# Optimization experiments

Hardware: AMD Instinct MI355X
Metric: run time of the kernel (lower is better)

The kernel has to match this reference:

```python
import jax, jax.numpy as jnp
import numpy as np
import math

B, L, D_MODEL = 4, 2048, 512
EXPAND, D_STATE, D_CONV = 6, 8, 3
D_INNER = EXPAND * D_MODEL            # 3072
DT_RANK = math.ceil(D_MODEL / 16)     # 32
NH = 8
HF = D_MODEL // NH                    # 64


def setup_inputs() -> dict:
    key = jax.random.key(0)
    ks = jax.random.split(key, 16)
    n = lambda k, sh, s=0.02: jax.random.normal(k, sh, dtype=jnp.float32) * s
    return {
        "x": jax.random.normal(ks[0], (B, L, D_MODEL), dtype=jnp.float32),
        "norm_w": jnp.ones((D_MODEL,), jnp.float32),
        "in_proj_w": n(ks[1], (2 * D_INNER, D_MODEL)),
        "conv_w": n(ks[2], (D_INNER, 1, D_CONV), 0.2),
        "conv_b": jnp.zeros((D_INNER,), jnp.float32),
        "x_proj_w": n(ks[3], (DT_RANK + 2 * D_STATE, D_INNER)),
        "dt_head_w": n(ks[4], (D_INNER, DT_RANK)),
        "dt_head_b": jnp.zeros((D_INNER,), jnp.float32),
        "D": jnp.ones((D_INNER,), jnp.float32),
        "reduce_w": n(ks[5], (D_MODEL, D_INNER)),
        "q_net_w": n(ks[6], (D_MODEL, D_MODEL)),
        "gain_q_w": n(ks[7], (D_MODEL, D_MODEL)),
        "gain_k_w": n(ks[8], (D_MODEL, D_MODEL)),
        "alpha": jnp.ones((1,), jnp.float32),
        "beta": jnp.zeros((1,), jnp.float32),
        "qkv_w": n(ks[9], (3 * D_MODEL + NH, D_MODEL)),
        "qkv_b": jnp.zeros((3 * D_MODEL + NH,), jnp.float32),
        "ttt_lr_bias": jnp.zeros((NH,), jnp.float32),
        "W1": n(ks[10], (NH, HF, HF)),
        "b1": jnp.zeros((NH, HF), jnp.float32),
        "token_idx": 1.0 / jnp.arange(1, L + 1, dtype=jnp.float32),
        "token_idx_bias": jnp.zeros((L,), jnp.float32),
        "ttt_ln_w": jnp.ones((NH, HF), jnp.float32),
        "ttt_ln_b": jnp.zeros((NH, HF), jnp.float32),
        "post_norm_w": jnp.ones((D_MODEL,), jnp.float32),
        "post_norm_b": jnp.zeros((D_MODEL,), jnp.float32),
        "wo_w": n(ks[11], (D_MODEL, D_MODEL)),
        "wo_b": jnp.zeros((D_MODEL,), jnp.float32),
    }


def _rmsnorm(x, w, eps=1e-5):
    return x * jax.lax.rsqrt(jnp.mean(x * x, axis=-1, keepdims=True) + eps) * w


def _layernorm(x, w, b, eps=1e-5):
    mu = x.mean(-1, keepdims=True)
    xh = (x - mu) * jax.lax.rsqrt(x.var(-1, keepdims=True) + eps)
    return xh * w + b


def _longhorn_scan(x, z, dt, k, q, dt_b, D):
    # x,z,dt: [B,L,di]; k,q: [B,L,ds].  Online Longhorn recurrence (matches step()).
    def step(s, t):
        x_t, z_t, dt_t, k_t, q_t = t
        dt_t = jax.nn.sigmoid(dt_t + dt_b)
        dt_t = dt_t / (1.0 + dt_t * jnp.sum(k_t * k_t, -1, keepdims=True))
        dB = dt_t[:, :, None] * k_t[:, None, :]                  # [B,di,ds]
        s = s * (1.0 - dB * k_t[:, None, :]) + x_t[:, :, None] * dB
        y_t = jnp.einsum('bdn,bn->bd', s, q_t) + D * x_t
        return s, y_t * jax.nn.silu(z_t)

    s0 = jnp.zeros((x.shape[0], x.shape[2], k.shape[2]), x.dtype)
    xs = tuple(jnp.moveaxis(a, 1, 0) for a in (x, z, dt, k, q))
    _, ys = jax.lax.scan(step, s0, xs)
    return jnp.moveaxis(ys, 0, 1)                                # [B,L,di]


def _ttt(h, qkv_w, qkv_b, ttt_lr_bias, W1, b1, token_idx, token_idx_bias,
         ln_w, ln_b, pn_w, pn_b, wo_w, wo_b, lr_mult=1.0):
    Bh, N, d = h.shape
    proj = h @ qkv_w.T + qkv_b                                   # [B,N,3d+NH]
    XQK, XV, XGate, lr = (proj[..., :d], proj[..., d:2 * d],
                          proj[..., 2 * d:3 * d], proj[..., 3 * d:])

    def heads(a):  # [B,N,d] -> [B*NH,N,HF]
        return a.reshape(Bh, N, NH, HF).transpose(0, 2, 1, 3).reshape(Bh * NH, N, HF)

    XQ = heads(XQK)            # XQ == XK in the source
    XVh = heads(XV)
    ttt_lr = jax.nn.sigmoid(lr + ttt_lr_bias) * lr_mult          # [B,N,NH]
    ttt_lr = jnp.swapaxes(ttt_lr, 0, 1).reshape(N, Bh * NH, 1)   # [N,B*NH,1]
    tok = jnp.maximum(token_idx + token_idx_bias, 0.0)           # [N]

    W1c = jnp.broadcast_to(W1[None], (Bh, NH, HF, HF)).reshape(Bh * NH, HF, HF)
    b1c = jnp.broadcast_to(b1[None], (Bh, NH, HF)).reshape(Bh * NH, HF)
    lnw = jnp.broadcast_to(ln_w[None], (Bh, NH, HF)).reshape(Bh * NH, HF)
    lnb = jnp.broadcast_to(ln_b[None], (Bh, NH, HF)).reshape(Bh * NH, HF)
    eps = 1e-6
    HFf = jnp.float32(HF)

    def step(carry, t):
        W, bb = carry
        xk, xv, lr_t, tok_t = t
        Z1 = jnp.einsum('bf,bfg->bg', xk, W) + bb
        mu = Z1.mean(-1, keepdims=True)
        std = jnp.sqrt(Z1.var(-1, keepdims=True) + eps)
        xh = (Z1 - mu) / std
        # grad of ||LN(Z1) - (XV - XK)||^2 wrt Z1 (ln_fused_l2_bwd)
        go = (lnw * xh + lnb) - (xv - xk)
        gxh = go * lnw
        grad = (HFf * gxh - gxh.sum(-1, keepdims=True)
                - xh * (gxh * xh).sum(-1, keepdims=True)) / (HFf * std)
        eta = lr_t * tok_t                                       # [B*NH,1]
        W = W - eta[:, :, None] * (xk[:, :, None] * grad[:, None, :])
        bb = bb - eta * grad
        Z1q = jnp.einsum('bf,bfg->bg', xk, W) + bb
        mu2 = Z1q.mean(-1, keepdims=True)
        std2 = jnp.sqrt(Z1q.var(-1, keepdims=True) + eps)
        out_t = xk + lnw * (Z1q - mu2) / std2 + lnb
        return (W, bb), out_t

    xs = (jnp.moveaxis(XQ, 1, 0), jnp.moveaxis(XVh, 1, 0), ttt_lr, tok)
    _, ys = jax.lax.scan(step, (W1c, b1c), xs)                   # [N,B*NH,HF]
    xqw = ys.reshape(N, Bh, NH, HF).transpose(1, 0, 2, 3).reshape(Bh, N, d)
    normed = _layernorm(xqw, pn_w, pn_b)
    gated = jax.nn.gelu(XGate, approximate=True) * normed
    return gated @ wo_w.T + wo_b


def reference(x, norm_w, in_proj_w, conv_w, conv_b, x_proj_w, dt_head_w, dt_head_b,
              D, reduce_w, q_net_w, gain_q_w, gain_k_w, alpha, beta,
              qkv_w, qkv_b, ttt_lr_bias, W1, b1, token_idx, token_idx_bias,
              ttt_ln_w, ttt_ln_b, post_norm_w, post_norm_b, wo_w, wo_b):
    residual = x                                   # residual=None in forward
    xn = _rmsnorm(residual, norm_w)
    # ---- Longhorn block ----
    xz = xn @ in_proj_w.T                          # [B,L,2*di]
    xx, z = jnp.split(xz, 2, axis=-1)
    xc = jnp.swapaxes(xx, 1, 2)                    # [B,di,L]
    xc = jax.lax.conv_general_dilated(
        xc, conv_w, (1,), [(D_CONV - 1, 0)],       # causal depthwise conv
        dimension_numbers=('NCH', 'OIH', 'NCH'), feature_group_count=D_INNER)
    xc = jax.nn.silu(xc + conv_b[None, :, None])
    xb = jnp.swapaxes(xc, 1, 2)                    # [B,L,di]
    x_dbl = xb @ x_proj_w.T
    dt = x_dbl[..., :DT_RANK] @ dt_head_w.T        # [B,L,di] (bias added in scan)
    k = x_dbl[..., DT_RANK:DT_RANK + D_STATE]
    q = x_dbl[..., DT_RANK + D_STATE:]
    y = _longhorn_scan(xb, z, dt, k, q, dt_head_b, D)   # h_hidden, [B,L,di]
    # (out_proj output is discarded by PreCoBlock, so not computed)
    h_red = y @ reduce_w.T                          # [B,L,d]
    # ---- TTT corrective branch ----
    c_hidden = _ttt(h_red, qkv_w, qkv_b, ttt_lr_bias, W1, b1, token_idx,
                    token_idx_bias, ttt_ln_w, ttt_ln_b, post_norm_w, post_norm_b,
                    wo_w, wo_b, lr_mult=1.0)
    z_long = h_red @ q_net_w.T
    z_ttt = c_hidden @ q_net_w.T
    gq = h_red @ gain_q_w.T
    gk = h_red @ gain_k_w.T
    # score = mean_i (gq_i . gk_j)/sqrt(d) == (mean_i gq_i) . gk_j / sqrt(d)
    score = jnp.einsum('bd,bld->bl', gq.mean(axis=1), gk) / jnp.sqrt(jnp.float32(D_MODEL))
    gain = jnp.minimum(jax.nn.sigmoid(alpha * score + beta), 0.55)[..., None]
    out = z_long + gain * (z_ttt - z_long)
    return (out, residual, gain)
```

## Files before the change

### kernel.cpp

```cpp
#include <hip/hip_runtime.h>
#include <hip/hip_bf16.h>
#include <cstdint>
#include <cstddef>

#define L_SEQ 2048
#define BATCH 4
#define DM    512
#define DI    3072
#define NROWS (BATCH * L_SEQ)
#define PROJW 1544
#define CTILE 16
#define BDI   (BATCH * DI)
#define SB    64
#define NSB   (L_SEQ / SB)
#define CHT   16
#define LCH   128
#define NLCH  (L_SEQ / LCH)

using bf16 = __hip_bfloat16;

typedef __attribute__((ext_vector_type(8))) short short8v;
typedef __attribute__((ext_vector_type(4))) float f32x4;


__device__ __forceinline__ float sigmoidf_(float x) { return 1.f / (1.f + __expf(-x)); }
__device__ __forceinline__ float us2f(unsigned int u) {
    union { unsigned int i; float f; } c; c.i = u << 16; return c.f;
}
__device__ __forceinline__ bf16  f2b(float f) { return __float2bfloat16(f); }
__device__ __forceinline__ float b2f(bf16 v)  { return __bfloat162float(v); }
__device__ __forceinline__ void st1(float* p, float v) { *p = v; }
__device__ __forceinline__ void st1(bf16* p, float v)  { *p = f2b(v); }

template <int CTRL>
__device__ __forceinline__ float dppadd_(float x) {
    int s = __builtin_amdgcn_update_dpp(0, __builtin_bit_cast(int, x), CTRL, 0xF, 0xF, true);
    return x + __builtin_bit_cast(float, s);
}
__device__ __forceinline__ float wave_sum_u(float x) {
    x = dppadd_<0x111>(x);
    x = dppadd_<0x112>(x);
    x = dppadd_<0x114>(x);
    x = dppadd_<0x118>(x);
    x = dppadd_<0x142>(x);
    x = dppadd_<0x143>(x);
    return __builtin_bit_cast(float,
        __builtin_amdgcn_readlane(__builtin_bit_cast(int, x), 63));
}

__global__ __launch_bounds__(256) void copy4_k(const float4* __restrict__ in,
                                               float4* __restrict__ out, int n) {
    int i = blockIdx.x * 256 + threadIdx.x;
    if (i < n) out[i] = in[i];
}

__global__ __launch_bounds__(256) void cvt_k(const float* __restrict__ in,
                                             bf16* __restrict__ out, int n4) {
    int i = blockIdx.x * 256 + threadIdx.x;
    if (i >= n4) return;
    float4 v = ((const float4*)in)[i];
    out[4 * i + 0] = f2b(v.x);
    out[4 * i + 1] = f2b(v.y);
    out[4 * i + 2] = f2b(v.z);
    out[4 * i + 3] = f2b(v.w);
}

__global__ __launch_bounds__(256) void cvt3_k(const float* __restrict__ a,
                                              const float* __restrict__ b,
                                              const float* __restrict__ c,
                                              bf16* __restrict__ out) {
    int i = blockIdx.x * 256 + threadIdx.x;
    const int seg = 512 * 512 / 4;
    const float* src = (i < seg) ? a : (i < 2 * seg) ? b : c;
    int j = (i < seg) ? i : (i < 2 * seg) ? i - seg : i - 2 * seg;
    float4 v = ((const float4*)src)[j];
    bf16* o = out + (size_t)i * 4;
    o[0] = f2b(v.x); o[1] = f2b(v.y); o[2] = f2b(v.z); o[3] = f2b(v.w);
}

__global__ __launch_bounds__(256) void rmsnorm_res_k(const float* __restrict__ x,
                                                     const float* __restrict__ w,
                                                     bf16* __restrict__ xn,
                                                     float* __restrict__ res) {
    int r = blockIdx.x, tid = threadIdx.x;
    const float* row = x + (size_t)r * DM;
    float v0 = row[tid], v1 = row[tid + 256];
    float q = v0 * v0 + v1 * v1;
#pragma unroll
    for (int off = 32; off; off >>= 1) q += __shfl_xor(q, off);
    __shared__ float sm[4];
    if ((tid & 63) == 0) sm[tid >> 6] = q;
    __syncthreads();
    q = sm[0] + sm[1] + sm[2] + sm[3];
    float scale = rsqrtf(q * (1.f / 512.f) + 1e-5f);
    bf16* orow = xn + (size_t)r * DM;
    float* rrow = res + (size_t)r * DM;
    orow[tid]       = f2b(v0 * scale * w[tid]);
    orow[tid + 256] = f2b(v1 * scale * w[tid + 256]);
    rrow[tid]       = v0;
    rrow[tid + 256] = v1;
}

template <int BIAS, typename TC>
__global__ __launch_bounds__(256) void gemm_mfma(const bf16* __restrict__ A, int lda,
                                                 const bf16* __restrict__ Wb, int ldw,
                                                 const float* __restrict__ bias,
                                                 TC* __restrict__ C, int ldc,
                                                 int N, int K) {
    __shared__ __align__(16) bf16 As[128 * 48];
    __shared__ __align__(16) bf16 Ws[128 * 48];
    const int tid = threadIdx.x;
    const int lane = tid & 63;
    const int widx = tid >> 6;
    const int bm = blockIdx.x * 128;
    const int bn = blockIdx.y * 128;
    const int wr = (widx >> 1) * 64;
    const int wc = (widx & 1) * 64;

    f32x4 acc[4][4];
#pragma unroll
    for (int i = 0; i < 4; ++i)
#pragma unroll
        for (int j = 0; j < 4; ++j) acc[i][j] = (f32x4){0.f, 0.f, 0.f, 0.f};

    const int r0 = tid >> 2;
    const int c0 = tid & 3;
    const int frow = lane & 15;
    const int fk = (lane >> 4) * 8;

    int n0 = bn + r0;       if (n0 > N - 1) n0 = N - 1;
    int n1 = bn + r0 + 64;  if (n1 > N - 1) n1 = N - 1;
    const bf16* pa0 = A + (size_t)(bm + r0) * lda + c0 * 8;
    const bf16* pa1 = A + (size_t)(bm + r0 + 64) * lda + c0 * 8;
    const bf16* pb0 = Wb + (size_t)n0 * ldw + c0 * 8;
    const bf16* pb1 = Wb + (size_t)n1 * ldw + c0 * 8;

    for (int k0 = 0; k0 < K; k0 += 32) {
        short8v a0 = *(const short8v*)(pa0 + k0);
        short8v a1 = *(const short8v*)(pa1 + k0);
        short8v b0 = *(const short8v*)(pb0 + k0);
        short8v b1 = *(const short8v*)(pb1 + k0);
        __syncthreads();
        *(short8v*)&As[r0 * 48 + c0 * 8] = a0;
        *(short8v*)&As[(r0 + 64) * 48 + c0 * 8] = a1;
        *(short8v*)&Ws[r0 * 48 + c0 * 8] = b0;
        *(short8v*)&Ws[(r0 + 64) * 48 + c0 * 8] = b1;
        __syncthreads();
        short8v af[4], bg[4];
#pragma unroll
        for (int mi = 0; mi < 4; ++mi)
            af[mi] = *(const short8v*)&As[(wr + mi * 16 + frow) * 48 + fk];
#pragma unroll
        for (int ni = 0; ni < 4; ++ni)
            bg[ni] = *(const short8v*)&Ws[(wc + ni * 16 + frow) * 48 + fk];
#pragma unroll
        for (int mi = 0; mi < 4; ++mi)
#pragma unroll
            for (int ni = 0; ni < 4; ++ni)
                acc[mi][ni] = __builtin_amdgcn_mfma_f32_16x16x32_bf16(
                    af[mi], bg[ni], acc[mi][ni], 0, 0, 0);
    }

#pragma unroll
    for (int ni = 0; ni < 4; ++ni) {
        int col = bn + wc + ni * 16 + (lane & 15);
        if (col < N) {
            float bz = BIAS ? bias[col] : 0.f;
#pragma unroll
            for (int mi = 0; mi < 4; ++mi) {
                int rbase = bm + wr + mi * 16 + (lane >> 4) * 4;
#pragma unroll
                for (int r = 0; r < 4; ++r) {
                    float v = acc[mi][ni][r] + bz;
                    st1(&C[(size_t)(rbase + r) * ldc + col], v);
                }
            }
        }
    }
}

__global__ __launch_bounds__(256) void conv_boundary_k(const bf16* __restrict__ x,
                                                       bf16* __restrict__ side) {
    int idx = blockIdx.x * 256 + threadIdx.x;
    const int total = (L_SEQ / CTILE - 1) * 2 * BDI;
    if (idx >= total) return;
    int col = idx % BDI;
    int rr = idx / BDI;
    int tile = (rr >> 1) + 1;
    int r = rr & 1;
    int b = col / DI, d = col % DI;
    int l = tile * CTILE - 2 + r;
    side[idx] = x[((size_t)b * L_SEQ + l) * DI + d];
}

__global__ __launch_bounds__(256) void conv_tile_k(bf16* __restrict__ x,
                                                   const bf16* __restrict__ side,
                                                   const float* __restrict__ cw,
                                                   const float* __restrict__ cb) {
    int idx = blockIdx.x * 256 + threadIdx.x;
    const int total = (L_SEQ / CTILE) * BDI;
    if (idx >= total) return;
    int col = idx % BDI;
    int tile = idx / BDI;
    int b = col / DI, d = col % DI;
    float w0 = cw[3 * d], w1 = cw[3 * d + 1], w2 = cw[3 * d + 2], bias = cb[d];
    size_t base = ((size_t)b * L_SEQ + tile * CTILE) * DI + d;
    float xm2, xm1;
    if (tile == 0) { xm2 = 0.f; xm1 = 0.f; }
    else {
        const bf16* sp = side + ((size_t)(tile - 1) * 2) * BDI + col;
        xm2 = b2f(sp[0]);
        xm1 = b2f(sp[BDI]);
    }
    float cur = b2f(x[base]);
#pragma unroll
    for (int i = 0; i < CTILE; ++i) {
        float nxt = (i + 1 < CTILE) ? b2f(x[base + (size_t)(i + 1) * DI]) : 0.f;
        float a = bias + w0 * xm2 + w1 * xm1 + w2 * cur;
        x[base + (size_t)i * DI] = f2b(a * sigmoidf_(a));
        xm2 = xm1; xm1 = cur; cur = nxt;
    }
}

__global__ __launch_bounds__(256) void longhorn_p1(const bf16* __restrict__ xb,
                                                   const float* __restrict__ xdbl,
                                                   const float* __restrict__ dtw,
                                                   const float* __restrict__ dtb_v,
                                                   float* __restrict__ pq) {
    int idx = blockIdx.x * 256 + threadIdx.x;
    int ch = idx / BDI;
    int col = idx % BDI;
    int b = col / DI, d = col % DI;
    float w32[32];
#pragma unroll
    for (int i = 0; i < 32; ++i) w32[i] = dtw[d * 32 + i];
    float dtb = dtb_v[d];
    float P[8] = {1.f, 1.f, 1.f, 1.f, 1.f, 1.f, 1.f, 1.f};
    float Q[8] = {0.f, 0.f, 0.f, 0.f, 0.f, 0.f, 0.f, 0.f};
    size_t rbase = ((size_t)b * L_SEQ + ch * LCH) * DI + d;
    const float* xdb = xdbl + ((size_t)b * L_SEQ + ch * LCH) * 48;

    float xv = b2f(xb[rbase]);
    for (int t = 0; t < LCH; ++t) {
        float x_c = xv;
        if (t + 1 < LCH) xv = b2f(xb[rbase + (size_t)(t + 1) * DI]);
        const float* row = xdb + (size_t)t * 48;
        float dt_c = 0.f;
#pragma unroll
        for (int i = 0; i < 32; i += 4) {
            float4 r4 = *(const float4*)(row + i);
            dt_c = fmaf(r4.x, w32[i + 0], dt_c);
            dt_c = fmaf(r4.y, w32[i + 1], dt_c);
            dt_c = fmaf(r4.z, w32[i + 2], dt_c);
            dt_c = fmaf(r4.w, w32[i + 3], dt_c);
        }
        float kq[8];
#pragma unroll
        for (int i = 0; i < 8; i += 4) *(float4*)&kq[i] = *(const float4*)(row + 32 + i);
        float sig = sigmoidf_(dt_c + dtb);
        float ksq = 0.f;
#pragma unroll
        for (int n = 0; n < 8; ++n) ksq = fmaf(kq[n], kq[n], ksq);
        float dts = sig / (1.f + sig * ksq);
#pragma unroll
        for (int n = 0; n < 8; ++n) {
            float dB = dts * kq[n];
            float a = 1.f - dB * kq[n];
            P[n] *= a;
            Q[n] = fmaf(Q[n], a, x_c * dB);
        }
    }
    float* o = pq + (size_t)idx * 16;
#pragma unroll
    for (int n = 0; n < 8; n += 4) {
        *(float4*)(o + n)     = make_float4(P[n], P[n + 1], P[n + 2], P[n + 3]);
        *(float4*)(o + 8 + n) = make_float4(Q[n], Q[n + 1], Q[n + 2], Q[n + 3]);
    }
}

__global__ __launch_bounds__(256) void longhorn_p2(float* __restrict__ pq) {
    int col = blockIdx.x * 256 + threadIdx.x;
    float s[8] = {0.f, 0.f, 0.f, 0.f, 0.f, 0.f, 0.f, 0.f};
    for (int c = 0; c < NLCH; ++c) {
        float* base = pq + ((size_t)c * BDI + col) * 16;
        float P[8], Q[8];
#pragma unroll
        for (int n = 0; n < 8; n += 4) {
            *(float4*)&P[n] = *(const float4*)(base + n);
            *(float4*)&Q[n] = *(const float4*)(base + 8 + n);
        }
#pragma unroll
        for (int n = 0; n < 8; n += 4)
            *(float4*)(base + n) = make_float4(s[n], s[n + 1], s[n + 2], s[n + 3]);
#pragma unroll
        for (int n = 0; n < 8; ++n) s[n] = fmaf(P[n], s[n], Q[n]);
    }
}

__global__ __launch_bounds__(256) void longhorn_p3(bf16* __restrict__ xb_y,
                                                   const bf16* __restrict__ z,
                                                   const float* __restrict__ xdbl,
                                                   const float* __restrict__ dtw,
                                                   const float* __restrict__ dtb_v,
                                                   const float* __restrict__ Dv,
                                                   const float* __restrict__ pq) {
    int idx = blockIdx.x * 256 + threadIdx.x;
    int ch = idx / BDI;
    int col = idx % BDI;
    int b = col / DI, d = col % DI;
    float w32[32];
#pragma unroll
    for (int i = 0; i < 32; ++i) w32[i] = dtw[d * 32 + i];
    float dtb = dtb_v[d], Dd = Dv[d];
    float s[8];
    {
        const float* base = pq + (size_t)idx * 16;
#pragma unroll
        for (int n = 0; n < 8; n += 4) *(float4*)&s[n] = *(const float4*)(base + n);
    }
    size_t rbase = ((size_t)b * L_SEQ + ch * LCH) * DI + d;
    const float* xdb = xdbl + ((size_t)b * L_SEQ + ch * LCH) * 48;

    float xv = b2f(xb_y[rbase]);
    float zv = b2f(z[rbase]);
    for (int t = 0; t < LCH; ++t) {
        float x_c = xv, z_c = zv;
        if (t + 1 < LCH) {
            size_t nidx = rbase + (size_t)(t + 1) * DI;
            xv = b2f(xb_y[nidx]);
            zv = b2f(z[nidx]);
        }
        const float* row = xdb + (size_t)t * 48;
        float dt_c = 0.f;
#pragma unroll
        for (int i = 0; i < 32; i += 4) {
            float4 r4 = *(const float4*)(row + i);
            dt_c = fmaf(r4.x, w32[i + 0], dt_c);
            dt_c = fmaf(r4.y, w32[i + 1], dt_c);
            dt_c = fmaf(r4.z, w32[i + 2], dt_c);
            dt_c = fmaf(r4.w, w32[i + 3], dt_c);
        }
        float kq[16];
#pragma unroll
        for (int i = 0; i < 16; i += 4) *(float4*)&kq[i] = *(const float4*)(row + 32 + i);
        float sig = sigmoidf_(dt_c + dtb);
        float ksq = 0.f;
#pragma unroll
        for (int n = 0; n < 8; ++n) ksq = fmaf(kq[n], kq[n], ksq);
        float dts = sig / (1.f + sig * ksq);
        float y = 0.f;
#pragma unroll
        for (int n = 0; n < 8; ++n) {
            float dB = dts * kq[n];
            s[n] = s[n] * (1.f - dB * kq[n]) + x_c * dB;
            y = fmaf(s[n], kq[8 + n], y);
        }
        y = fmaf(Dd, x_c, y);
        float out = y * (z_c * sigmoidf_(z_c));
        xb_y[rbase + (size_t)t * DI] = f2b(out);
    }
}

__global__ __launch_bounds__(128) void prep_ttt_k(const bf16* __restrict__ proj,
                                                  const float* __restrict__ lr_bias,
                                                  const float* __restrict__ tok_idx,
                                                  const float* __restrict__ tok_bias,
                                                  const float* __restrict__ ln_w,
                                                  const float* __restrict__ ln_b,
                                                  float* __restrict__ xkf,
                                                  float* __restrict__ etav,
                                                  float* __restrict__ q0s) {
    int bh = blockIdx.x >> 4;
    int t = (blockIdx.x & 15) * 128 + threadIdx.x;
    int b = bh >> 3, h = bh & 7;
    const bf16* prow = proj + ((size_t)b * L_SEQ + t) * PROJW;
    const bf16* pk = prow + h * 64;
    const bf16* pv = prow + 512 + h * 64;
    const float* lwp = ln_w + h * 64;
    const float* lbp = ln_b + h * 64;
    float* xo = xkf + ((size_t)bh * L_SEQ + t) * 64;
    float q0 = 0.f;
#pragma unroll
    for (int i = 0; i < 64; i += 8) {
        short8v sk = *(const short8v*)(pk + i);
        short8v sv = *(const short8v*)(pv + i);
        float v[8];
#pragma unroll
        for (int j = 0; j < 8; ++j) {
            float xk = us2f((unsigned short)sk[j]);
            float xv = us2f((unsigned short)sv[j]);
            v[j] = xk;
            q0 = fmaf((lbp[i + j] - xv + xk), lwp[i + j], q0);
        }
        *(float4*)(xo + i)     = make_float4(v[0], v[1], v[2], v[3]);
        *(float4*)(xo + i + 4) = make_float4(v[4], v[5], v[6], v[7]);
    }
    float eta = sigmoidf_(b2f(prow[1536 + h]) + lr_bias[h]) *
                fmaxf(tok_idx[t] + tok_bias[t], 0.f);
    size_t o = (size_t)bh * L_SEQ + t;
    etav[o] = eta;
    q0s[o]  = q0;
}

__global__ __launch_bounds__(64) void gram16_k(const float* __restrict__ xkf,
                                               float* __restrict__ gram) {
    int bh = blockIdx.x >> 7, c16 = blockIdx.x & 127;
    int lane = threadIdx.x;
    __shared__ __align__(16) float xs[16][68];
    const float* src = xkf + ((size_t)bh * L_SEQ + c16 * 16) * 64;
    {
        int r = lane >> 2, cb = (lane & 3) * 16;
#pragma unroll
        for (int j = 0; j < 4; ++j)
            *(float4*)&xs[r][cb + 4 * j] = *(const float4*)(src + (size_t)r * 64 + cb + 4 * j);
    }
    __syncthreads();
    int t = lane >> 2, s0 = lane & 3;
    float* dst = gram + ((size_t)(bh * 128 + c16) * 16 + t) * 16;
#pragma unroll
    for (int jj = 0; jj < 4; ++jj) {
        int s = s0 * 4 + jj;
        float a0 = 0.f, a1 = 0.f, a2 = 0.f, a3 = 0.f;
#pragma unroll
        for (int j = 0; j < 16; ++j) {
            float4 u = *(const float4*)&xs[t][4 * j];
            float4 v = *(const float4*)&xs[s][4 * j];
            a0 = fmaf(u.x, v.x, a0); a1 = fmaf(u.y, v.y, a1);
            a2 = fmaf(u.z, v.z, a2); a3 = fmaf(u.w, v.w, a3);
        }
        dst[s] = (a0 + a1) + (a2 + a3);
    }
}

__device__ __forceinline__ void ttt_body(const bf16* __restrict__ proj,
                                         const float* __restrict__ xkf,
                                         const float* __restrict__ etav,
                                         const float* __restrict__ q0s,
                                         const float* __restrict__ gram16,
                                         const float* __restrict__ W1,
                                         const float* __restrict__ b1,
                                         const float* __restrict__ ln_w,
                                         const float* __restrict__ ln_b,
                                         bf16* __restrict__ xqw) {
    const int lane = threadIdx.x;
    const int bh = blockIdx.x;
    const int b = bh >> 3, h = bh & 7;

    __shared__ __align__(16) float xkb[2][SB][64];
    __shared__ __align__(16) bf16  xvb[2][SB][64];
    __shared__ __align__(16) float kb[2][4][CHT][CHT];
    __shared__ __align__(16) float sc[2][2][SB];
    __shared__ __align__(16) float zbb[CHT][64];
    __shared__ __align__(16) float z1qb[CHT][64];
    __shared__ __align__(16) float egb[CHT][64];
    __shared__ float mub[CHT];

    float W[64];
#pragma unroll
    for (int f = 0; f < 64; ++f) W[f] = W1[(size_t)(h * 64 + f) * 64 + lane];
    float bvec = b1[h * 64 + lane];
    float lw = ln_w[h * 64 + lane];
    float lb = ln_b[h * 64 + lane];
    float p = lw * lw;

    const float* kfg = xkf + (size_t)bh * L_SEQ * 64;
    const bf16*  pvg = proj + (size_t)b * L_SEQ * PROJW + 512 + h * 64;
    const float* evg = etav + (size_t)bh * L_SEQ;
    const float* qg  = q0s + (size_t)bh * L_SEQ;
    const float* gmg = gram16 + (size_t)bh * 128 * 256;

    auto stage_async = [&](int c, int bi) {
        const int t0g = c * SB;
#pragma unroll
        for (int i = 0; i < 16; ++i) {
            const float* gp = kfg + (size_t)(t0g + 4 * i) * 64 + lane * 4;
            __builtin_amdgcn_global_load_lds(
                (const __attribute__((address_space(1))) void*)gp,
                (__attribute__((address_space(3))) void*)&xkb[bi][4 * i][0], 16, 0, 0);
        }
#pragma unroll
        for (int i = 0; i < 8; ++i) {
            const bf16* gp = pvg + (size_t)(t0g + 8 * i + (lane >> 3)) * PROJW + (lane & 7) * 8;
            __builtin_amdgcn_global_load_lds(
                (const __attribute__((address_space(1))) void*)gp,
                (__attribute__((address_space(3))) void*)&xvb[bi][8 * i][0], 16, 0, 0);
        }
#pragma unroll
        for (int i = 0; i < 4; ++i) {
            const float* gp = gmg + (size_t)c * 1024 + i * 256 + lane * 4;
            __builtin_amdgcn_global_load_lds(
                (const __attribute__((address_space(1))) void*)gp,
                (__attribute__((address_space(3))) void*)(&kb[bi][0][0][0] + i * 256), 16, 0, 0);
        }
        {
            const float* g0 = evg + t0g + lane;
            __builtin_amdgcn_global_load_lds(
                (const __attribute__((address_space(1))) void*)g0,
                (__attribute__((address_space(3))) void*)&sc[bi][0][0], 4, 0, 0);
            const float* g1 = qg + t0g + lane;
            __builtin_amdgcn_global_load_lds(
                (const __attribute__((address_space(1))) void*)g1,
                (__attribute__((address_space(3))) void*)&sc[bi][1][0], 4, 0, 0);
        }
    };
    auto matvec16 = [&](int nbuf, int nt0) {
#pragma unroll 4
        for (int t = 0; t < CHT; ++t) {
            const float4* row = (const float4*)&xkb[nbuf][nt0 + t][0];
            float a0 = 0.f, a1 = 0.f, a2 = 0.f, a3 = 0.f;
#pragma unroll
            for (int j = 0; j < 16; ++j) {
                float4 kv = row[j];
                a0 = fmaf(kv.x, W[4 * j + 0], a0);
                a1 = fmaf(kv.y, W[4 * j + 1], a1);
                a2 = fmaf(kv.z, W[4 * j + 2], a2);
                a3 = fmaf(kv.w, W[4 * j + 3], a3);
            }
            float zb = (a0 + a1) + (a2 + a3) + bvec;
            zbb[t][lane] = zb;
            float m = wave_sum_u(zb) * 0.015625f;
            if (lane == 0) mub[t] = m;
        }
    };

    stage_async(0, 0);
    asm volatile("s_waitcnt vmcnt(0)" ::: "memory");
    __builtin_amdgcn_sched_barrier(0);
    matvec16(0, 0);

    bf16* xq = xqw + ((size_t)b * L_SEQ) * DM + h * 64 + lane;

    for (int c = 0; c < NSB; ++c) {
        const int cur = c & 1;
        if (c + 1 < NSB) stage_async(c + 1, 1 - cur);
#pragma unroll 1
        for (int sub = 0; sub < 4; ++sub) {
            const int t0 = sub * CHT;
            float eg[CHT];
            float bacc = 0.f;
            float4 krA, krB, krC, krD;
            {
                const float4* krow = (const float4*)&kb[cur][sub][0][0];
                krA = krow[0]; krB = krow[1]; krC = krow[2]; krD = krow[3];
            }
            float zb_n = zbb[0][lane];
            float xk_n = xkb[cur][t0 + 0][lane];
            float xv_n = b2f(xvb[cur][t0 + 0][lane]);
            float et_n = sc[cur][0][t0 + 0];
            float q0_n = sc[cur][1][t0 + 0];
            float mu_n = mub[0];
#pragma unroll
            for (int t = 0; t < CHT; ++t) {
                float kr[CHT];
                *(float4*)&kr[0]  = krA;
                *(float4*)&kr[4]  = krB;
                *(float4*)&kr[8]  = krC;
                *(float4*)&kr[12] = krD;
                float zb_v = zb_n;
                float xk_c = xk_n;
                float xv_c = xv_n;
                float eta  = et_n;
                float q0u  = q0_n;
                float muv  = mu_n;
                if (t + 1 < CHT) {
                    const float4* krow = (const float4*)&kb[cur][sub][t + 1][0];
                    krA = krow[0]; krB = krow[1]; krC = krow[2]; krD = krow[3];
                    zb_n = zbb[t + 1][lane];
                    xk_n = xkb[cur][t0 + t + 1][lane];
                    xv_n = b2f(xvb[cur][t0 + t + 1][lane]);
                    et_n = sc[cur][0][t0 + t + 1];
                    q0_n = sc[cur][1][t0 + t + 1];
                    mu_n = mub[t + 1];
                }

                float gg0 = bacc, gg1 = 0.f, gg2 = 0.f, gg3 = 0.f;
#pragma unroll
                for (int s = 0; s < t; ++s) {
                    if ((s & 3) == 0) gg0 = fmaf(kr[s], eg[s], gg0);
                    else if ((s & 3) == 1) gg1 = fmaf(kr[s], eg[s], gg1);
                    else if ((s & 3) == 2) gg2 = fmaf(kr[s], eg[s], gg2);
                    else gg3 = fmaf(kr[s], eg[s], gg3);
                }
                float z1 = zb_v - ((gg0 + gg1) + (gg2 + gg3));
// ... 119 lines not shown
            bg[ni] = *(const short8v*)&Ws[(wc + ni * 16 + frow) * 48 + fk];
#pragma unroll
        for (int mi = 0; mi < 4; ++mi)
#pragma unroll
            for (int ni = 0; ni < 4; ++ni)
                acc[mi][ni] = __builtin_amdgcn_mfma_f32_16x16x32_bf16(
                    af[mi], bg[ni], acc[mi][ni], 0, 0, 0);
    }

#pragma unroll
    for (int ni = 0; ni < 4; ++ni) {
        int col = bn + wc + ni * 16 + (lane & 15);
        int buf = col >> 9;
        int lc = col & 511;
        bf16* Cb = (buf == 0) ? zl : (buf == 1) ? gq : gk;
#pragma unroll
        for (int mi = 0; mi < 4; ++mi) {
            int rbase = bm + wr + mi * 16 + (lane >> 4) * 4;
#pragma unroll
            for (int r = 0; r < 4; ++r)
                Cb[(size_t)(rbase + r) * 512 + lc] = f2b(acc[mi][ni][r]);
        }
    }
}

__global__ __launch_bounds__(256) void gated_k(const bf16* __restrict__ xqw,
                                               const bf16* __restrict__ proj,
                                               const float* __restrict__ pnw,
                                               const float* __restrict__ pnb,
                                               bf16* __restrict__ gated) {
    int r = blockIdx.x, tid = threadIdx.x;
    const bf16* row = xqw + (size_t)r * DM;
    float v0 = b2f(row[tid]), v1 = b2f(row[tid + 256]);
    float s = v0 + v1, q = v0 * v0 + v1 * v1;
#pragma unroll
    for (int off = 32; off; off >>= 1) {
        s += __shfl_xor(s, off);
        q += __shfl_xor(q, off);
    }
    __shared__ float sm[8];
    if ((tid & 63) == 0) { sm[tid >> 6] = s; sm[4 + (tid >> 6)] = q; }
    __syncthreads();
    s = sm[0] + sm[1] + sm[2] + sm[3];
    q = sm[4] + sm[5] + sm[6] + sm[7];
    float mu = s * (1.f / 512.f);
    float var = q * (1.f / 512.f) - mu * mu;
    float istd = rsqrtf(var + 1e-5f);
    const bf16* grow = proj + (size_t)r * PROJW + 1024;
    bf16* orow = gated + (size_t)r * DM;
#pragma unroll
    for (int e = 0; e < 2; ++e) {
        int c = tid + e * 256;
        float xv = (e == 0) ? v0 : v1;
        float nv = (xv - mu) * istd * pnw[c] + pnb[c];
        float g = b2f(grow[c]);
        float gg = 0.5f * g * (1.f + tanhf(0.7978845608028654f * (g + 0.044715f * g * g * g)));
        orow[c] = f2b(gg * nv);
    }
}

__global__ __launch_bounds__(256) void mean1_k(const bf16* __restrict__ gq,
                                               float* __restrict__ partial) {
    int blk = blockIdx.x;
    int b = blk >> 4, c = blk & 15;
    int tid = threadIdx.x;
    const bf16* p = gq + ((size_t)b * L_SEQ + c * 128) * DM + tid * 2;
    float a0 = 0.f, a1 = 0.f;
    for (int l = 0; l < 128; ++l) {
        ushort2 u = *(const ushort2*)(p + (size_t)l * DM);
        a0 += us2f(u.x); a1 += us2f(u.y);
    }
    partial[(size_t)blk * DM + tid * 2]     = a0;
    partial[(size_t)blk * DM + tid * 2 + 1] = a1;
}
__global__ __launch_bounds__(256) void mean2_k(const float* __restrict__ partial,
                                               float* __restrict__ gqm) {
    int t = blockIdx.x * 256 + threadIdx.x;
    if (t >= 2048) return;
    int b = t >> 9, d = t & 511;
    float acc = 0.f;
#pragma unroll
    for (int c = 0; c < 16; ++c) acc += partial[(size_t)(b * 16 + c) * DM + d];
    gqm[t] = acc * (1.f / 2048.f);
}

__global__ __launch_bounds__(64) void final_k(const bf16* __restrict__ zl,
                                              const bf16* __restrict__ zt,
                                              const bf16* __restrict__ gk,
                                              const float* __restrict__ gqm,
                                              const float* __restrict__ alpha,
                                              const float* __restrict__ beta,
                                              float* __restrict__ out,
                                              float* __restrict__ gain_out) {
    int r = blockIdx.x;
    int lane = threadIdx.x;
    int b = r >> 11;
    const bf16* gkr = gk + (size_t)r * DM;
    const float* gmb = gqm + b * DM;
    float acc = 0.f;
#pragma unroll
    for (int i = 0; i < 8; ++i) acc = fmaf(gmb[lane + 64 * i], b2f(gkr[lane + 64 * i]), acc);
#pragma unroll
    for (int off = 32; off; off >>= 1) acc += __shfl_xor(acc, off);
    float score = acc * 0.04419417382415922f;
    float g = sigmoidf_(alpha[0] * score + beta[0]);
    g = fminf(g, 0.55f);
    if (lane == 0) gain_out[r] = g;
    const bf16* zlr = zl + (size_t)r * DM;
    const bf16* ztr = zt + (size_t)r * DM;
    float* orow = out + (size_t)r * DM;
#pragma unroll
    for (int i = 0; i < 8; ++i) {
        int c = lane + 64 * i;
        float a = b2f(zlr[c]);
        orow[c] = a + g * (b2f(ztr[c]) - a);
    }
}


extern "C" void kernel_launch(void* const* d_in, const int* in_sizes, int n_in,
                              void* d_out, int out_size, void* d_ws, size_t ws_size,
                              hipStream_t stream) {
    const float* x           = (const float*)d_in[0];
    const float* norm_w      = (const float*)d_in[1];
    const float* in_proj_w   = (const float*)d_in[2];
    const float* conv_w      = (const float*)d_in[3];
    const float* conv_b      = (const float*)d_in[4];
    const float* x_proj_w    = (const float*)d_in[5];
    const float* dt_head_w   = (const float*)d_in[6];
    const float* dt_head_b   = (const float*)d_in[7];
    const float* Dvec        = (const float*)d_in[8];
    const float* reduce_w    = (const float*)d_in[9];
    const float* q_net_w     = (const float*)d_in[10];
    const float* gain_q_w    = (const float*)d_in[11];
    const float* gain_k_w    = (const float*)d_in[12];
    const float* alpha       = (const float*)d_in[13];
    const float* beta        = (const float*)d_in[14];
    const float* qkv_w       = (const float*)d_in[15];
    const float* qkv_b       = (const float*)d_in[16];
    const float* ttt_lr_bias = (const float*)d_in[17];
    const float* W1          = (const float*)d_in[18];
    const float* b1          = (const float*)d_in[19];
    const float* token_idx   = (const float*)d_in[20];
    const float* token_bias  = (const float*)d_in[21];
    const float* ttt_ln_w    = (const float*)d_in[22];
    const float* ttt_ln_b    = (const float*)d_in[23];
    const float* post_norm_w = (const float*)d_in[24];
    const float* post_norm_b = (const float*)d_in[25];
    const float* wo_w        = (const float*)d_in[26];
    const float* wo_b        = (const float*)d_in[27];

    const size_t SZ_ROWDM = (size_t)NROWS * DM;
    const size_t MB = 1024u * 1024u;
    char* base = (char*)d_ws;

    float* out_p  = (float*)d_out;
    float* res_p  = out_p + SZ_ROWDM;
    float* gain_p = out_p + 2 * SZ_ROWDM;

    if (ws_size < 116 * MB) {
        copy4_k<<<(int)(SZ_ROWDM / 4 / 256), 256, 0, stream>>>(
            (const float4*)x, (float4*)res_p, (int)(SZ_ROWDM / 4));
        return;
    }

    bf16*  ws0   = (bf16*)base;
    bf16*  wcat  = (bf16*)base;
    bf16*  wob16 = (bf16*)(base + 2 * MB);
    bf16*  xn    = (bf16*)(base + 7 * MB);
    bf16*  h_red = xn;
    bf16*  cside = (bf16*)(base + 7 * MB);
    float* lpq   = (float*)base;
    bf16*  bufX  = (bf16*)(base + 16 * MB);
    bf16*  bufZ  = (bf16*)(base + 64 * MB);
    float* xdbl  = (float*)(base + 112 * MB);
    float* gqm   = (float*)(base + 113 * MB + 512 * 1024);
    float* mpart = (float*)(base + 114 * MB);
    bf16*  proj  = bufX;
    bf16*  xqw   = bufZ;
    bf16*  zl    = (bf16*)(base + 72 * MB);
    bf16*  gq    = (bf16*)(base + 80 * MB);
    float* gramb = (float*)(base + 88 * MB);
    bf16*  gk    = (bf16*)(base + 92 * MB);
    bf16*  zttt  = (bf16*)(base + 100 * MB);
    bf16*  gated = (bf16*)(base + 104 * MB);
    bf16*  chid  = (bf16*)(base + 42 * MB);
    float* xkf   = (float*)(base + 42 * MB);
    float* etav  = (float*)(base + 58 * MB);
    float* q0s   = (float*)(base + 58 * MB + 512 * 1024);

    rmsnorm_res_k<<<NROWS, 256, 0, stream>>>(x, norm_w, xn, res_p);

    cvt_k<<<(2 * DI * DM / 4 + 255) / 256, 256, 0, stream>>>(in_proj_w, ws0, 2 * DI * DM / 4);
    {
        dim3 g(NROWS / 128, DI / 128);
        gemm_mfma<0, bf16><<<g, 256, 0, stream>>>(xn, DM, ws0, DM, nullptr, bufX, DI, DI, DM);
        gemm_mfma<0, bf16><<<g, 256, 0, stream>>>(xn, DM, ws0 + (size_t)DI * DM, DM, nullptr, bufZ, DI, DI, DM);
    }

    conv_boundary_k<<<((L_SEQ / CTILE - 1) * 2 * BDI) / 256, 256, 0, stream>>>(bufX, cside);
    conv_tile_k<<<((L_SEQ / CTILE) * BDI) / 256, 256, 0, stream>>>(bufX, cside, conv_w, conv_b);

    cvt_k<<<(48 * DI / 4 + 255) / 256, 256, 0, stream>>>(x_proj_w, ws0, 48 * DI / 4);
    {
        dim3 g(NROWS / 128, 1);
        gemm_mfma<0, float><<<g, 256, 0, stream>>>(bufX, DI, ws0, DI, nullptr, xdbl, 48, 48, DI);
    }

    longhorn_p1<<<(NLCH * BDI) / 256, 256, 0, stream>>>(bufX, xdbl, dt_head_w, dt_head_b, lpq);
    longhorn_p2<<<BDI / 256, 256, 0, stream>>>(lpq);
    longhorn_p3<<<(NLCH * BDI) / 256, 256, 0, stream>>>(bufX, bufZ, xdbl, dt_head_w,
                                                        dt_head_b, Dvec, lpq);

    cvt_k<<<(DM * DI / 4 + 255) / 256, 256, 0, stream>>>(reduce_w, ws0, DM * DI / 4);
    {
        dim3 g(NROWS / 128, DM / 128);
        gemm_mfma<0, bf16><<<g, 256, 0, stream>>>(bufX, DI, ws0, DI, nullptr, h_red, DM, DM, DI);
    }

    cvt_k<<<(PROJW * DM / 4 + 255) / 256, 256, 0, stream>>>(qkv_w, ws0, PROJW * DM / 4);
    {
        dim3 g(NROWS / 128, (PROJW + 127) / 128);
        gemm_mfma<1, bf16><<<g, 256, 0, stream>>>(h_red, DM, ws0, DM, qkv_b, proj, PROJW, PROJW, DM);
    }

    prep_ttt_k<<<32 * 16, 128, 0, stream>>>(proj, ttt_lr_bias, token_idx, token_bias,
                                            ttt_ln_w, ttt_ln_b, xkf, etav, q0s);
    gram16_k<<<32 * 128, 64, 0, stream>>>(xkf, gramb);
    cvt3_k<<<3 * 256, 256, 0, stream>>>(q_net_w, gain_q_w, gain_k_w, wcat);

    hetero_k<<<32 + 768, 256, 0, stream>>>(proj, xkf, etav, q0s, gramb, W1, b1,
                                           ttt_ln_w, ttt_ln_b, xqw,
                                           h_red, wcat, zl, gq, gk);

    gated_k<<<NROWS, 256, 0, stream>>>(xqw, proj, post_norm_w, post_norm_b, gated);

    cvt_k<<<(DM * DM / 4 + 255) / 256, 256, 0, stream>>>(wo_w, wob16, DM * DM / 4);
    {
        dim3 g(NROWS / 128, DM / 128);
        gemm_mfma<1, bf16><<<g, 256, 0, stream>>>(gated, DM, wob16, DM, wo_b, chid, DM, DM, DM);
        gemm_mfma<0, bf16><<<g, 256, 0, stream>>>(chid, DM, wcat, DM, nullptr, zttt, DM, DM, DM);
    }

    mean1_k<<<64, 256, 0, stream>>>(gq, mpart);
    mean2_k<<<8, 256, 0, stream>>>(mpart, gqm);
    final_k<<<NROWS, 64, 0, stream>>>(zl, zttt, gk, gqm, alpha, beta, out_p, gain_p);
}
```

Baseline: 2.304 ms.

## Fuse weight conversions, merge in_proj GEMMs, fuse gram into prep, enlarge scan chunk

Merges all weight fp32-to-bf16 conversions into a single launch writing to separate buffers, and merges the two in_proj GEMMs into one specialized kernel with a doubled grid that routes tiles to the x or z output. Computes the 16x16 Gram blocks inside the TTT prep kernel from shared memory instead of rereading xkf in a separate kernel. Doubles the Longhorn scan chunk length, which halves the number of chunks and the parallelism of the chunked scan passes. The intent is to cut launch count and redundant global traffic, at the cost of a new workspace layout that must not alias live buffers.

```diff
diff --git a/kernel.cpp b/kernel.cpp
--- a/kernel.cpp
+++ b/kernel.cpp
@@ -14,7 +14,7 @@
 #define SB    64
 #define NSB   (L_SEQ / SB)
 #define CHT   16
-#define LCH   128
+#define LCH   256
 #define NLCH  (L_SEQ / LCH)
 
 using bf16 = __hip_bfloat16;
@@ -65,16 +65,37 @@
     out[4 * i + 3] = f2b(v.w);
 }
 
-__global__ __launch_bounds__(256) void cvt3_k(const float* __restrict__ a,
-                                              const float* __restrict__ b,
-                                              const float* __restrict__ c,
-                                              bf16* __restrict__ out) {
+#define C_RED  393216
+#define C_QKV  197632
+#define C_WO   65536
+#define C_XP   73728
+#define C_W1   65536
+__global__ __launch_bounds__(256) void cvt_all_k(const float* __restrict__ reduce_w,
+                                                 const float* __restrict__ qkv_w,
+                                                 const float* __restrict__ wo_w,
+                                                 const float* __restrict__ xproj_w,
+                                                 const float* __restrict__ qnet_w,
+                                                 const float* __restrict__ gainq_w,
+                                                 const float* __restrict__ gaink_w,
+                                                 bf16* __restrict__ redb,
+                                                 bf16* __restrict__ qkvb,
+                                                 bf16* __restrict__ wob,
+                                                 bf16* __restrict__ xpb,
+                                                 bf16* __restrict__ wcat) {
     int i = blockIdx.x * 256 + threadIdx.x;
-    const int seg = 512 * 512 / 4;
-    const float* src = (i < seg) ? a : (i < 2 * seg) ? b : c;
-    int j = (i < seg) ? i : (i < 2 * seg) ? i - seg : i - 2 * seg;
+    const float* src;
+    bf16* dst;
+    int j;
+    if (i < C_RED)                { src = reduce_w; dst = redb;  j = i; }
+    else if (i < C_RED + C_QKV)   { src = qkv_w;    dst = qkvb;  j = i - C_RED; }
+    else if (i < C_RED + C_QKV + C_WO) { src = wo_w; dst = wob;  j = i - C_RED - C_QKV; }
+    else if (i < C_RED + C_QKV + C_WO + C_XP) { src = xproj_w; dst = xpb; j = i - C_RED - C_QKV - C_WO; }
+    else if (i < C_RED + C_QKV + C_WO + C_XP + C_W1) { src = qnet_w; dst = wcat; j = i - C_RED - C_QKV - C_WO - C_XP; }
+    else if (i < C_RED + C_QKV + C_WO + C_XP + 2 * C_W1) { src = gainq_w; dst = wcat + (size_t)C_W1 * 4; j = i - C_RED - C_QKV - C_WO - C_XP - C_W1; }
+    else if (i < C_RED + C_QKV + C_WO + C_XP + 3 * C_W1) { src = gaink_w; dst = wcat + (size_t)2 * C_W1 * 4; j = i - C_RED - C_QKV - C_WO - C_XP - 2 * C_W1; }
+    else return;
     float4 v = ((const float4*)src)[j];
-    bf16* o = out + (size_t)i * 4;
+    bf16* o = dst + (size_t)j * 4;
     o[0] = f2b(v.x); o[1] = f2b(v.y); o[2] = f2b(v.z); o[3] = f2b(v.w);
 }
 
@@ -175,6 +196,77 @@
                     st1(&C[(size_t)(rbase + r) * ldc + col], v);
                 }
             }
+        }
+    }
+}
+
+__global__ __launch_bounds__(256) void gemm_inproj(const bf16* __restrict__ A,
+                                                   const bf16* __restrict__ Wb,
+                                                   bf16* __restrict__ cx,
+                                                   bf16* __restrict__ cz) {
+    __shared__ __align__(16) bf16 As[128 * 48];
+    __shared__ __align__(16) bf16 Ws[128 * 48];
+    const int tid = threadIdx.x;
+    const int lane = tid & 63;
+    const int widx = tid >> 6;
+    const int bm = blockIdx.x * 128;
+    const int bn = blockIdx.y * 128;
+    const int wr = (widx >> 1) * 64;
+    const int wc = (widx & 1) * 64;
+
+    f32x4 acc[4][4];
+#pragma unroll
+    for (int i = 0; i < 4; ++i)
+#pragma unroll
+        for (int j = 0; j < 4; ++j) acc[i][j] = (f32x4){0.f, 0.f, 0.f, 0.f};
+
+    const int r0 = tid >> 2;
+    const int c0 = tid & 3;
+    const int frow = lane & 15;
+    const int fk = (lane >> 4) * 8;
+
+    const bf16* pa0 = A + (size_t)(bm + r0) * DM + c0 * 8;
+    const bf16* pa1 = A + (size_t)(bm + r0 + 64) * DM + c0 * 8;
+    const bf16* pb0 = Wb + (size_t)(bn + r0) * DM + c0 * 8;
+    const bf16* pb1 = Wb + (size_t)(bn + r0 + 64) * DM + c0 * 8;
+
+    for (int k0 = 0; k0 < DM; k0 += 32) {
+        short8v a0 = *(const short8v*)(pa0 + k0);
+        short8v a1 = *(const short8v*)(pa1 + k0);
+        short8v b0 = *(const short8v*)(pb0 + k0);
+        short8v b1 = *(const short8v*)(pb1 + k0);
+        __syncthreads();
+        *(short8v*)&As[r0 * 48 + c0 * 8] = a0;
+        *(short8v*)&As[(r0 + 64) * 48 + c0 * 8] = a1;
+        *(short8v*)&Ws[r0 * 48 + c0 * 8] = b0;
+        *(short8v*)&Ws[(r0 + 64) * 48 + c0 * 8] = b1;
+        __syncthreads();
+        short8v af[4], bg[4];
+#pragma unroll
+        for (int mi = 0; mi < 4; ++mi)
+            af[mi] = *(const short8v*)&As[(wr + mi * 16 + frow) * 48 + fk];
+#pragma unroll
+        for (int ni = 0; ni < 4; ++ni)
+            bg[ni] = *(const short8v*)&Ws[(wc + ni * 16 + frow) * 48 + fk];
+#pragma unroll
+        for (int mi = 0; mi < 4; ++mi)
+#pragma unroll
+            for (int ni = 0; ni < 4; ++ni)
+                acc[mi][ni] = __builtin_amdgcn_mfma_f32_16x16x32_bf16(
+                    af[mi], bg[ni], acc[mi][ni], 0, 0, 0);
+    }
+
+    bf16* Cb = (bn < DI) ? cx : cz;
+    const int coff = (bn < DI) ? 0 : DI;
+#pragma unroll
+    for (int ni = 0; ni < 4; ++ni) {
+        int col = bn + wc + ni * 16 + (lane & 15) - coff;
+#pragma unroll
+        for (int mi = 0; mi < 4; ++mi) {
+            int rbase = bm + wr + mi * 16 + (lane >> 4) * 4;
+#pragma unroll
+            for (int r = 0; r < 4; ++r)
+                Cb[(size_t)(rbase + r) * DI + col] = f2b(acc[mi][ni][r]);
         }
     }
 }
@@ -361,17 +453,21 @@
     }
 }
 
-__global__ __launch_bounds__(128) void prep_ttt_k(const bf16* __restrict__ proj,
-                                                  const float* __restrict__ lr_bias,
-                                                  const float* __restrict__ tok_idx,
-                                                  const float* __restrict__ tok_bias,
-                                                  const float* __restrict__ ln_w,
-                                                  const float* __restrict__ ln_b,
-                                                  float* __restrict__ xkf,
-                                                  float* __restrict__ etav,
-                                                  float* __restrict__ q0s) {
+__global__ __launch_bounds__(128) void prep_gram_k(const bf16* __restrict__ proj,
+                                                   const float* __restrict__ lr_bias,
+                                                   const float* __restrict__ tok_idx,
+                                                   const float* __restrict__ tok_bias,
+                                                   const float* __restrict__ ln_w,
+                                                   const float* __restrict__ ln_b,
+                                                   float* __restrict__ xkf,
+                                                   float* __restrict__ etav,
+                                                   float* __restrict__ q0s,
+                                                   float* __restrict__ gram) {
+    __shared__ __align__(16) float xs[128][68];
     int bh = blockIdx.x >> 4;
-    int t = (blockIdx.x & 15) * 128 + threadIdx.x;
+    int blk16 = blockIdx.x & 15;
+    int tid = threadIdx.x;
+    int t = blk16 * 128 + tid;
     int b = bh >> 3, h = bh & 7;
     const bf16* prow = proj + ((size_t)b * L_SEQ + t) * PROJW;
     const bf16* pk = prow + h * 64;
@@ -392,43 +488,34 @@
             v[j] = xk;
             q0 = fmaf((lbp[i + j] - xv + xk), lwp[i + j], q0);
         }
-        *(float4*)(xo + i)     = make_float4(v[0], v[1], v[2], v[3]);
-        *(float4*)(xo + i + 4) = make_float4(v[4], v[5], v[6], v[7]);
+        float4 lo = make_float4(v[0], v[1], v[2], v[3]);
+        float4 hi = make_float4(v[4], v[5], v[6], v[7]);
+        *(float4*)(xo + i)     = lo;
+        *(float4*)(xo + i + 4) = hi;
+        *(float4*)&xs[tid][i]     = lo;
+        *(float4*)&xs[tid][i + 4] = hi;
     }
     float eta = sigmoidf_(b2f(prow[1536 + h]) + lr_bias[h]) *
                 fmaxf(tok_idx[t] + tok_bias[t], 0.f);
     size_t o = (size_t)bh * L_SEQ + t;
     etav[o] = eta;
     q0s[o]  = q0;
-}
-
-__global__ __launch_bounds__(64) void gram16_k(const float* __restrict__ xkf,
-                                               float* __restrict__ gram) {
-    int bh = blockIdx.x >> 7, c16 = blockIdx.x & 127;
-    int lane = threadIdx.x;
-    __shared__ __align__(16) float xs[16][68];
-    const float* src = xkf + ((size_t)bh * L_SEQ + c16 * 16) * 64;
-    {
-        int r = lane >> 2, cb = (lane & 3) * 16;
-#pragma unroll
-        for (int j = 0; j < 4; ++j)
-            *(float4*)&xs[r][cb + 4 * j] = *(const float4*)(src + (size_t)r * 64 + cb + 4 * j);
-    }
     __syncthreads();
-    int t = lane >> 2, s0 = lane & 3;
-    float* dst = gram + ((size_t)(bh * 128 + c16) * 16 + t) * 16;
-#pragma unroll
-    for (int jj = 0; jj < 4; ++jj) {
-        int s = s0 * 4 + jj;
+    int chunk = tid >> 4, tt = tid & 15;
+    const float* rt = &xs[chunk * 16 + tt][0];
+    float* dst = gram + (((size_t)bh * 128 + blk16 * 8 + chunk) * 16 + tt) * 16;
+#pragma unroll
+    for (int ss = 0; ss < 16; ++ss) {
+        const float* rs = &xs[chunk * 16 + ss][0];
         float a0 = 0.f, a1 = 0.f, a2 = 0.f, a3 = 0.f;
 #pragma unroll
         for (int j = 0; j < 16; ++j) {
-            float4 u = *(const float4*)&xs[t][4 * j];
-            float4 v = *(const float4*)&xs[s][4 * j];
+            float4 u = *(const float4*)(rt + 4 * j);
+            float4 v = *(const float4*)(rs + 4 * j);
             a0 = fmaf(u.x, v.x, a0); a1 = fmaf(u.y, v.y, a1);
             a2 = fmaf(u.z, v.z, a2); a3 = fmaf(u.w, v.w, a3);
         }
-        dst[s] = (a0 + a1) + (a2 + a3);
+        dst[ss] = (a0 + a1) + (a2 + a3);
     }
 }
 
@@ -854,6 +941,7 @@
 
     const size_t SZ_ROWDM = (size_t)NROWS * DM;
     const size_t MB = 1024u * 1024u;
+    const size_t KB = 1024u;
     char* base = (char*)d_ws;
 
     float* out_p  = (float*)d_out;
@@ -866,47 +954,52 @@
         return;
     }
 
-    bf16*  ws0   = (bf16*)base;
-    bf16*  wcat  = (bf16*)base;
-    bf16*  wob16 = (bf16*)(base + 2 * MB);
-    bf16*  xn    = (bf16*)(base + 7 * MB);
-    bf16*  h_red = xn;
-    bf16*  cside = (bf16*)(base + 7 * MB);
-    float* lpq   = (float*)base;
-    bf16*  bufX  = (bf16*)(base + 16 * MB);
-    bf16*  bufZ  = (bf16*)(base + 64 * MB);
-    float* xdbl  = (float*)(base + 112 * MB);
-    float* gqm   = (float*)(base + 113 * MB + 512 * 1024);
-    float* mpart = (float*)(base + 114 * MB);
-    bf16*  proj  = bufX;
-    bf16*  xqw   = bufZ;
-    bf16*  zl    = (bf16*)(base + 72 * MB);
-    bf16*  gq    = (bf16*)(base + 80 * MB);
-    float* gramb = (float*)(base + 88 * MB);
-    bf16*  gk    = (bf16*)(base + 92 * MB);
-    bf16*  zttt  = (bf16*)(base + 100 * MB);
-    bf16*  gated = (bf16*)(base + 104 * MB);
-    bf16*  chid  = (bf16*)(base + 42 * MB);
-    float* xkf   = (float*)(base + 42 * MB);
-    float* etav  = (float*)(base + 58 * MB);
-    float* q0s   = (float*)(base + 58 * MB + 512 * 1024);
+    bf16*  ws0    = (bf16*)base;
+    bf16*  redb   = (bf16*)base;
+    bf16*  qkvb   = (bf16*)(base + 3 * MB);
+    bf16*  wob16  = (bf16*)(base + 4 * MB + 768 * KB);
+    bf16*  xpb    = (bf16*)(base + 5 * MB + 512 * KB);
+    bf16*  wcat   = (bf16*)(base + 114 * MB + 512 * KB);
+    bf16*  xn     = (bf16*)(base + 7 * MB);
+    bf16*  h_red  = xn;
+    bf16*  cside  = (bf16*)(base + 7 * MB);
+    float* lpq    = (float*)(base + 7 * MB);
+    bf16*  bufX   = (bf16*)(base + 16 * MB);
+    bf16*  bufZ   = (bf16*)(base + 64 * MB);
+    float* xdbl   = (float*)(base + 112 * MB);
+    float* gqm    = (float*)(base + 113 * MB + 512 * KB);
+    float* mpart  = (float*)(base + 114 * MB);
+    bf16*  proj   = bufX;
+    bf16*  xqw    = bufZ;
+    bf16*  zl     = (bf16*)(base + 72 * MB);
+    bf16*  gq     = (bf16*)(base + 80 * MB);
+    float* gramb  = (float*)(base + 88 * MB);
+    bf16*  gk     = (bf16*)(base + 92 * MB);
+    bf16*  zttt   = (bf16*)(base + 100 * MB);
+    bf16*  gated  = (bf16*)(base + 104 * MB);
+    bf16*  chid   = (bf16*)(base + 42 * MB);
+    float* xkf    = (float*)(base + 42 * MB);
+    float* etav   = (float*)(base + 58 * MB);
+    float* q0s    = (float*)(base + 58 * MB + 512 * KB);
 
     rmsnorm_res_k<<<NROWS, 256, 0, stream>>>(x, norm_w, xn, res_p);
 
     cvt_k<<<(2 * DI * DM / 4 + 255) / 256, 256, 0, stream>>>(in_proj_w, ws0, 2 * DI * DM / 4);
     {
-        dim3 g(NROWS / 128, DI / 128);
-        gemm_mfma<0, bf16><<<g, 256, 0, stream>>>(xn, DM, ws0, DM, nullptr, bufX, DI, DI, DM);
-        gemm_mfma<0, bf16><<<g, 256, 0, stream>>>(xn, DM, ws0 + (size_t)DI * DM, DM, nullptr, bufZ, DI, DI, DM);
-    }
+        dim3 g(NROWS / 128, 2 * DI / 128);
+        gemm_inproj<<<g, 256, 0, stream>>>(xn, ws0, bufX, bufZ);
+    }
+
+    cvt_all_k<<<(C_RED + C_QKV + C_WO + C_XP + 3 * C_W1 + 255) / 256, 256, 0, stream>>>(
+        reduce_w, qkv_w, wo_w, x_proj_w, q_net_w, gain_q_w, gain_k_w,
+        redb, qkvb, wob16, xpb, wcat);
 
     conv_boundary_k<<<((L_SEQ / CTILE - 1) * 2 * BDI) / 256, 256, 0, stream>>>(bufX, cside);
     conv_tile_k<<<((L_SEQ / CTILE) * BDI) / 256, 256, 0, stream>>>(bufX, cside, conv_w, conv_b);
 
-    cvt_k<<<(48 * DI / 4 + 255) / 256, 256, 0, stream>>>(x_proj_w, ws0, 48 * DI / 4);
     {
         dim3 g(NROWS / 128, 1);
-        gemm_mfma<0, float><<<g, 256, 0, stream>>>(bufX, DI, ws0, DI, nullptr, xdbl, 48, 48, DI);
+        gemm_mfma<0, float><<<g, 256, 0, stream>>>(bufX, DI, xpb, DI, nullptr, xdbl, 48, 48, DI);
     }
 
     longhorn_p1<<<(NLCH * BDI) / 256, 256, 0, stream>>>(bufX, xdbl, dt_head_w, dt_head_b, lpq);
@@ -914,22 +1007,18 @@
     longhorn_p3<<<(NLCH * BDI) / 256, 256, 0, stream>>>(bufX, bufZ, xdbl, dt_head_w,
                                                         dt_head_b, Dvec, lpq);
 
-    cvt_k<<<(DM * DI / 4 + 255) / 256, 256, 0, stream>>>(reduce_w, ws0, DM * DI / 4);
     {
         dim3 g(NROWS / 128, DM / 128);
-        gemm_mfma<0, bf16><<<g, 256, 0, stream>>>(bufX, DI, ws0, DI, nullptr, h_red, DM, DM, DI);
-    }
-
-    cvt_k<<<(PROJW * DM / 4 + 255) / 256, 256, 0, stream>>>(qkv_w, ws0, PROJW * DM / 4);
+        gemm_mfma<0, bf16><<<g, 256, 0, stream>>>(bufX, DI, redb, DI, nullptr, h_red, DM, DM, DI);
+    }
+
     {
         dim3 g(NROWS / 128, (PROJW + 127) / 128);
-        gemm_mfma<1, bf16><<<g, 256, 0, stream>>>(h_red, DM, ws0, DM, qkv_b, proj, PROJW, PROJW, DM);
-    }
-
-    prep_ttt_k<<<32 * 16, 128, 0, stream>>>(proj, ttt_lr_bias, token_idx, token_bias,
-                                            ttt_ln_w, ttt_ln_b, xkf, etav, q0s);
-    gram16_k<<<32 * 128, 64, 0, stream>>>(xkf, gramb);
-    cvt3_k<<<3 * 256, 256, 0, stream>>>(q_net_w, gain_q_w, gain_k_w, wcat);
+        gemm_mfma<1, bf16><<<g, 256, 0, stream>>>(h_red, DM, qkvb, DM, qkv_b, proj, PROJW, PROJW, DM);
+    }
+
+    prep_gram_k<<<32 * 16, 128, 0, stream>>>(proj, ttt_lr_bias, token_idx, token_bias,
+                                             ttt_ln_w, ttt_ln_b, xkf, etav, q0s, gramb);
 
     hetero_k<<<32 + 768, 256, 0, stream>>>(proj, xkf, etav, q0s, gramb, W1, b1,
                                            ttt_ln_w, ttt_ln_b, xqw,
@@ -937,7 +1026,6 @@
 
     gated_k<<<NROWS, 256, 0, stream>>>(xqw, proj, post_norm_w, post_norm_b, gated);
 
-    cvt_k<<<(DM * DM / 4 + 255) / 256, 256, 0, stream>>>(wo_w, wob16, DM * DM / 4);
     {
         dim3 g(NROWS / 128, DM / 128);
         gemm_mfma<1, bf16><<<g, 256, 0, stream>>>(gated, DM, wob16, DM, wo_b, chid, DM, DM, DM);
```

Measured after the change: 2.501 ms. 1.09x slower.
